# Kernel optimization log

Hardware: AMD Instinct MI355X
Metric: run time of the kernel (lower is better)

## Reference

```python
import jax, jax.numpy as jnp
import numpy as np
from jax import lax

NUM_GROUPS = 16
POOL_KS = 2
CLAMP_MIN = 0.0
CLAMP_MAX = 1.0
EPS = 1e-5


def setup_inputs() -> dict:
    key = jax.random.key(0)
    k1, k2, k3, k4, k5 = jax.random.split(key, 5)
    B, Cin, H, W = 32, 64, 128, 128
    Cout, K = 128, 3
    x = jax.random.normal(k1, (B, Cin, H, W), dtype=jnp.float32)
    fan_in = Cin * K * K
    bound = 1.0 / np.sqrt(fan_in)
    conv_w = jax.random.uniform(k2, (Cout, Cin, K, K), jnp.float32, -bound, bound)
    conv_b = jax.random.uniform(k3, (Cout,), jnp.float32, -bound, bound)
    gn_w = jnp.ones((Cout,), jnp.float32)
    gn_b = jnp.zeros((Cout,), jnp.float32)
    scale = jnp.ones((Cout, 1, 1), jnp.float32)
    return {"x": x, "conv_w": conv_w, "conv_b": conv_b,
            "gn_w": gn_w, "gn_b": gn_b, "scale": scale}


def reference(x, conv_w, conv_b, gn_w, gn_b, scale):
    # Conv2d, stride=1, padding=0  -> (B, Cout, Ho, Wo)
    y = lax.conv_general_dilated(
        x, conv_w, window_strides=(1, 1), padding="VALID",
        dimension_numbers=("NCHW", "OIHW", "NCHW"))
    y = y + conv_b[None, :, None, None]
    B, C, H, W = y.shape
    G = NUM_GROUPS
    # GroupNorm (biased variance, as in torch)
    yg = y.reshape(B, G, C // G, H, W)
    mean = jnp.mean(yg, axis=(2, 3, 4), keepdims=True)
    var = jnp.mean(jnp.square(yg), axis=(2, 3, 4), keepdims=True) - jnp.square(mean)
    yn = (yg - mean) * lax.rsqrt(var + EPS)
    yn = yn.reshape(B, C, H, W) * gn_w[None, :, None, None] + gn_b[None, :, None, None]
    # per-channel scale
    yn = yn * scale[None, :, :, :]
    # MaxPool2d(kernel=POOL_KS, stride=POOL_KS), VALID
    pooled = lax.reduce_window(
        yn, -jnp.inf, lax.max,
        window_dimensions=(1, 1, POOL_KS, POOL_KS),
        window_strides=(1, 1, POOL_KS, POOL_KS),
        padding="VALID")
    return jnp.clip(pooled, CLAMP_MIN, CLAMP_MAX)
```

## Files before the change

kernel.cpp:

```cpp
#include <hip/hip_runtime.h>
#include <stdint.h>
#include <stddef.h>

#define HIN 128
#define WIN 128
#define CINC 64
#define COUTC 128
#define HO 126
#define WO 126
#define HP 63
#define WP 63
#define NB 32
#define NG 16

typedef __bf16 bf16x8 __attribute__((ext_vector_type(8)));
typedef float f32x16 __attribute__((ext_vector_type(16)));

#define AS1U(p) ((const __attribute__((address_space(1))) unsigned int*)(p))
#define AS3U(p) ((__attribute__((address_space(3))) unsigned int*)(p))

__device__ __forceinline__ unsigned int f2bf(float f) {
  unsigned int u = __float_as_uint(f);
  return (u + 0x7fffu + ((u >> 16) & 1u)) >> 16;
}

__global__ __launch_bounds__(256) void wtrans_k(const float* __restrict__ w,
                                                unsigned short* __restrict__ wt2,
                                                float* __restrict__ stats) {
  int i = blockIdx.x * 256 + threadIdx.x;
  if (i < 1024) stats[i] = 0.0f;
  if (i >= 73728) return;
  int j = i & 7;
  int co = (i >> 3) & 127;
  int th = i >> 10;
  int half = th & 1, ks = (th >> 1) & 3, tap = th >> 3;
  int kh = tap / 3, kw = tap - 3 * kh;
  int cin = ks * 16 + half * 8 + j;
  float v = w[((co * CINC + cin) * 3 + kh) * 3 + kw];
  wt2[i] = (unsigned short)f2bf(v);
}

__global__ __launch_bounds__(256, 2) void conv_k(const float* __restrict__ x,
                                                 const unsigned short* __restrict__ wt2,
                                                 const float* __restrict__ conv_b,
                                                 float* __restrict__ out,
                                                 float* __restrict__ stats) {
  __shared__ __align__(16) unsigned int x_lds[18 * 18 * 32];
  __shared__ __align__(16) unsigned int aux_lds[8192];

  int t = threadIdx.x;
  int lane = t & 63, wave = t >> 6;
  int tw = blockIdx.x & 7, th = blockIdx.x >> 3;
  int b = blockIdx.y;
  int oh0 = th * 16, ow0 = tw * 16;
  int half = lane >> 5, m = lane & 31;

  int rot = (blockIdx.x + b) % 9;
  const unsigned int* wg = (const unsigned int*)wt2;

#define DMA_HALFTAP(j)                                                         \
  {                                                                            \
    int tapj = rot + ((j) >> 1);                                               \
    if (tapj >= 9) tapj -= 9;                                                  \
    int srcb = (tapj * 2 + ((j)&1)) * 2048;                                    \
    int slot = (j)&3;                                                          \
    _Pragma("unroll")                                                          \
    for (int jj = 0; jj < 2; ++jj) {                                           \
      int dof = jj * 1024 + wave * 256;                                        \
      __builtin_amdgcn_global_load_lds(AS1U(wg + srcb + dof + lane * 4),       \
                                       AS3U(&aux_lds[slot * 2048 + dof]), 16,  \
                                       0, 0);                                  \
    }                                                                          \
  }

  DMA_HALFTAP(0)
  DMA_HALFTAP(1)

  float bias[4];
#pragma unroll
  for (int nt = 0; nt < 4; ++nt) bias[nt] = conv_b[nt * 32 + m];

  const float* xb = x + (size_t)b * CINC * HIN * WIN;
#pragma unroll
  for (int k = 0; k < 12; ++k) {
    int i = k * 256 + t;
    if (i < 2880) {
      int c4 = i % 5;
      int j = i / 5;
      int p = j & 31;
      int r = j >> 5;
      int gr = oh0 + r;
      int gc0 = ow0 + c4 * 4;
      float4 v0 = make_float4(0.f, 0.f, 0.f, 0.f);
      float4 v1 = v0;
      if (gr < HIN && gc0 < WIN) {
        const float* base = xb + ((size_t)(2 * p) * HIN + gr) * WIN + gc0;
        v0 = *(const float4*)base;
        v1 = *(const float4*)(base + HIN * WIN);
      }
      float e0[4] = {v0.x, v0.y, v0.z, v0.w};
      float e1[4] = {v1.x, v1.y, v1.z, v1.w};
#pragma unroll
      for (int cc = 0; cc < 4; ++cc) {
        int c = c4 * 4 + cc;
        if (c < 18) {
          unsigned int d = f2bf(e0[cc]) | (f2bf(e1[cc]) << 16);
          x_lds[(r * 18 + c) * 32 + (p ^ ((c & 7) << 2))] = d;
        }
      }
    }
  }
  __syncthreads();

  f32x16 acc[2][4];
#pragma unroll
  for (int nt = 0; nt < 4; ++nt)
#pragma unroll
    for (int mt = 0; mt < 2; ++mt)
#pragma unroll
      for (int r = 0; r < 16; ++r) acc[mt][nt][r] = bias[nt];

  int prb = wave * 4 + (m >> 4);
  int pcc = m & 15;

#pragma unroll
  for (int i = 0; i < 18; ++i) {
    if (i + 2 < 18) DMA_HALFTAP(i + 2)

    int tap = rot + (i >> 1);
    if (tap >= 9) tap -= 9;
    int kh = (tap * 11) >> 5;
    int kw = tap - 3 * kh;
    int c = pcc + kw;
    int swz = (c & 7) << 2;
    int slot = i & 3;
    int hp = i & 1;
#pragma unroll
    for (int ks2 = 0; ks2 < 2; ++ks2) {
      int ks = hp * 2 + ks2;
      int ab = c * 32 + ((ks * 8 + half * 4) ^ swz);
      bf16x8 afr[2];
#pragma unroll
      for (int mt = 0; mt < 2; ++mt)
        afr[mt] = __builtin_bit_cast(
            bf16x8, *(const uint4*)&x_lds[(prb + mt * 2 + kh) * 576 + ab]);
      int wbase = slot * 2048 + ks2 * 1024 + half * 512 + m * 4;
      __builtin_amdgcn_s_setprio(1);
#pragma unroll
      for (int nt = 0; nt < 4; ++nt) {
        bf16x8 bfr =
            __builtin_bit_cast(bf16x8, *(const uint4*)&aux_lds[wbase + nt * 128]);
#pragma unroll
        for (int mt = 0; mt < 2; ++mt)
          acc[mt][nt] = __builtin_amdgcn_mfma_f32_32x32x16_bf16(
              afr[mt], bfr, acc[mt][nt], 0, 0, 0);
      }
      __builtin_amdgcn_s_setprio(0);
    }
    if (i < 16) {
      asm volatile("s_waitcnt vmcnt(2)" ::: "memory");
    } else if (i == 16) {
      asm volatile("s_waitcnt vmcnt(0)" ::: "memory");
    }
    if (i < 17) {
      __builtin_amdgcn_s_barrier();
      __builtin_amdgcn_sched_barrier(0);
    }
  }
#undef DMA_HALFTAP

  float s[4] = {0.f, 0.f, 0.f, 0.f}, qs[4] = {0.f, 0.f, 0.f, 0.f};
#pragma unroll
  for (int nt = 0; nt < 4; ++nt) {
#pragma unroll
    for (int mt = 0; mt < 2; ++mt) {
#pragma unroll
      for (int reg = 0; reg < 16; ++reg) {
        int c16 = (reg & 3) + 4 * half + 8 * ((reg >> 2) & 1);
        int r8 = wave * 4 + mt * 2 + (reg >> 3);
        if ((oh0 + r8) < HO && (ow0 + c16) < WO) {
          float v = acc[mt][nt][reg];
          s[nt] += v;
          qs[nt] += v * v;
        }
      }
    }
  }
#pragma unroll
  for (int nt = 0; nt < 4; ++nt) {
    float sv = s[nt], qv = qs[nt];
    sv += __shfl_xor(sv, 32);
    qv += __shfl_xor(qv, 32);
    sv += __shfl_down(sv, 4, 8);
    qv += __shfl_down(qv, 4, 8);
    sv += __shfl_down(sv, 2, 8);
    qv += __shfl_down(qv, 2, 8);
    sv += __shfl_down(sv, 1, 8);
    qv += __shfl_down(qv, 1, 8);
    if (half == 0 && (m & 7) == 0) {
      int g = nt * 4 + (m >> 3);
      atomicAdd(&stats[(b * NG + g) * 2 + 0], sv);
      atomicAdd(&stats[(b * NG + g) * 2 + 1], qv);
    }
  }

  __syncthreads();

#pragma unroll
  for (int nt = 0; nt < 4; ++nt) {
    int co = nt * 32 + m;
#pragma unroll
    for (int mt = 0; mt < 2; ++mt) {
      int oh2l = wave * 2 + mt;
#pragma unroll
      for (int i = 0; i < 4; ++i) {
        int r0 = 2 * i;
        int ow2l = (i & 1) + 2 * half + 4 * (i >> 1);
        float mx = fmaxf(fmaxf(acc[mt][nt][r0], acc[mt][nt][r0 + 1]),
                         fmaxf(acc[mt][nt][r0 + 8], acc[mt][nt][r0 + 9]));
        x_lds[co * 66 + oh2l * 8 + ow2l] = __float_as_uint(mx);
      }
    }
  }
  __syncthreads();

#pragma unroll
  for (int i = 0; i < 4; ++i) {
    int row = t * 4 + i;
    int co = row >> 3, oh2l = row & 7;
    int oh2 = th * 8 + oh2l;
    if (oh2 < HP) {
      const uint2* src = (const uint2*)&x_lds[co * 66 + oh2l * 8];
      uint2 d0 = src[0], d1 = src[1], d2 = src[2], d3 = src[3];
      unsigned int v[8] = {d0.x, d0.y, d1.x, d1.y, d2.x, d2.y, d3.x, d3.y};
      float* ob = out + ((size_t)(b * COUTC + co) * HP + oh2) * WP + tw * 8;
      int n = (tw == 7) ? 7 : 8;
#pragma unroll
      for (int e = 0; e < 8; ++e)
        if (e < n) ob[e] = __uint_as_float(v[e]);
    }
  }
}

__global__ __launch_bounds__(256) void fin_k(float* __restrict__ out,
                                             const float* __restrict__ stats,
                                             const float* __restrict__ gn_w,
                                             const float* __restrict__ gn_b,
                                             const float* __restrict__ scale) {
  const int plane = HP * WP;
  const float inv_cnt = 1.0f / (8.0f * HO * WO);
  int bc = blockIdx.x;
  int c = bc & 127, b = bc >> 7;
  int g = c >> 3;
  float su = stats[(b * NG + g) * 2 + 0];
  float sq = stats[(b * NG + g) * 2 + 1];
  float mean = su * inv_cnt;
  float var = fmaxf(sq * inv_cnt - mean * mean, 0.f);
  float rstd = rsqrtf(var + 1e-5f);
  float gw = gn_w[c], sc = scale[c];
  float A = rstd * gw * sc;
  float Bo = (gn_b[c] - mean * rstd * gw) * sc;

  float* p = out + (size_t)bc * plane;
  int t = threadIdx.x;
  int head = (4 - (bc & 3)) & 3;
  if (t < head) p[t] = fminf(fmaxf(fmaf(p[t], A, Bo), 0.0f), 1.0f);
  int n4 = (plane - head) >> 2;
  float4* p4 = (float4*)(p + head);
  for (int i = t; i < n4; i += 256) {
    float4 v = p4[i];
    v.x = fminf(fmaxf(fmaf(v.x, A, Bo), 0.0f), 1.0f);
    v.y = fminf(fmaxf(fmaf(v.y, A, Bo), 0.0f), 1.0f);
    v.z = fminf(fmaxf(fmaf(v.z, A, Bo), 0.0f), 1.0f);
    v.w = fminf(fmaxf(fmaf(v.w, A, Bo), 0.0f), 1.0f);
    p4[i] = v;
  }
  int done = head + (n4 << 2);
  int tail = plane - done;
  if (t < tail) p[done + t] = fminf(fmaxf(fmaf(p[done + t], A, Bo), 0.0f), 1.0f);
}

extern "C" void kernel_launch(void* const* d_in, const int* in_sizes, int n_in,
                              void* d_out, int out_size, void* d_ws, size_t ws_size,
                              hipStream_t stream) {
  const float* x      = (const float*)d_in[0];
  const float* conv_w = (const float*)d_in[1];
  const float* conv_b = (const float*)d_in[2];
  const float* gn_w   = (const float*)d_in[3];
  const float* gn_b   = (const float*)d_in[4];
  const float* scale  = (const float*)d_in[5];
  float* out = (float*)d_out;

  float* stats        = (float*)d_ws;
  unsigned short* wt2 = (unsigned short*)((char*)d_ws + 4096);

  wtrans_k<<<288, 256, 0, stream>>>(conv_w, wt2, stats);

  conv_k<<<dim3(64, NB), 256, 0, stream>>>(x, wt2, conv_b, out, stats);

  fin_k<<<4096, 256, 0, stream>>>(out, stats, gn_w, gn_b, scale);
}
```

Baseline: 379.4 us.

## Halve conv output tile height and split waves across channels for occupancy

Each conv block now covers an 8x16 output tile instead of 16x16. Its four waves are arranged as 2 row groups by 2 channel halves, so each wave accumulates 64 output channels instead of 128, and the grid doubles to 128x32 blocks. LDS per block shrinks (x tile of 10 rows, 4-slot weight ring at quarter-tap granularity with 36 pipeline steps) and launch bounds request 3 blocks per CU, aiming for higher occupancy and lower accumulator register pressure. The trade-offs are more halo re-reads of x, duplicated weight streaming per block, and a barrier on every one of the 36 steps.

```diff
diff --git a/kernel.cpp b/kernel.cpp
--- a/kernel.cpp
+++ b/kernel.cpp
@@ -40,51 +40,41 @@
   wt2[i] = (unsigned short)f2bf(v);
 }
 
-__global__ __launch_bounds__(256, 2) void conv_k(const float* __restrict__ x,
+__global__ __launch_bounds__(256, 3) void conv_k(const float* __restrict__ x,
                                                  const unsigned short* __restrict__ wt2,
                                                  const float* __restrict__ conv_b,
                                                  float* __restrict__ out,
                                                  float* __restrict__ stats) {
-  __shared__ __align__(16) unsigned int x_lds[18 * 18 * 32];
-  __shared__ __align__(16) unsigned int aux_lds[8192];
+  __shared__ __align__(16) unsigned int x_lds[10 * 18 * 32];
+  __shared__ __align__(16) unsigned int w_lds[4096];
 
   int t = threadIdx.x;
   int lane = t & 63, wave = t >> 6;
+  int wh = wave >> 1, wc = wave & 1;
   int tw = blockIdx.x & 7, th = blockIdx.x >> 3;
   int b = blockIdx.y;
-  int oh0 = th * 16, ow0 = tw * 16;
+  int oh0 = th * 8, ow0 = tw * 16;
   int half = lane >> 5, m = lane & 31;
-
-  int rot = (blockIdx.x + b) % 9;
+  int rot4 = (((int)blockIdx.x + b) % 9) * 4;
   const unsigned int* wg = (const unsigned int*)wt2;
 
-#define DMA_HALFTAP(j)                                                         \
-  {                                                                            \
-    int tapj = rot + ((j) >> 1);                                               \
-    if (tapj >= 9) tapj -= 9;                                                  \
-    int srcb = (tapj * 2 + ((j)&1)) * 2048;                                    \
-    int slot = (j)&3;                                                          \
-    _Pragma("unroll")                                                          \
-    for (int jj = 0; jj < 2; ++jj) {                                           \
-      int dof = jj * 1024 + wave * 256;                                        \
-      __builtin_amdgcn_global_load_lds(AS1U(wg + srcb + dof + lane * 4),       \
-                                       AS3U(&aux_lds[slot * 2048 + dof]), 16,  \
-                                       0, 0);                                  \
-    }                                                                          \
-  }
-
-  DMA_HALFTAP(0)
-  DMA_HALFTAP(1)
-
-  float bias[4];
-#pragma unroll
-  for (int nt = 0; nt < 4; ++nt) bias[nt] = conv_b[nt * 32 + m];
+#pragma unroll
+  for (int j = 0; j < 2; ++j) {
+    int rs = j + rot4;
+    if (rs >= 36) rs -= 36;
+    __builtin_amdgcn_global_load_lds(AS1U(wg + rs * 1024 + wave * 256 + lane * 4),
+                                     AS3U(&w_lds[j * 1024 + wave * 256]), 16, 0, 0);
+  }
+
+  float bias[2];
+#pragma unroll
+  for (int nt = 0; nt < 2; ++nt) bias[nt] = conv_b[wc * 64 + nt * 32 + m];
 
   const float* xb = x + (size_t)b * CINC * HIN * WIN;
 #pragma unroll
-  for (int k = 0; k < 12; ++k) {
+  for (int k = 0; k < 7; ++k) {
     int i = k * 256 + t;
-    if (i < 2880) {
+    if (i < 1600) {
       int c4 = i % 5;
       int j = i / 5;
       int p = j & 31;
@@ -112,72 +102,71 @@
   }
   __syncthreads();
 
-  f32x16 acc[2][4];
-#pragma unroll
-  for (int nt = 0; nt < 4; ++nt)
+  f32x16 acc[2][2];
+#pragma unroll
+  for (int nt = 0; nt < 2; ++nt)
 #pragma unroll
     for (int mt = 0; mt < 2; ++mt)
 #pragma unroll
       for (int r = 0; r < 16; ++r) acc[mt][nt][r] = bias[nt];
 
-  int prb = wave * 4 + (m >> 4);
+  int prb = wh * 4 + (m >> 4);
   int pcc = m & 15;
 
 #pragma unroll
-  for (int i = 0; i < 18; ++i) {
-    if (i + 2 < 18) DMA_HALFTAP(i + 2)
-
-    int tap = rot + (i >> 1);
-    if (tap >= 9) tap -= 9;
+  for (int j = 0; j < 36; ++j) {
+    if (j + 2 < 36) {
+      int rs2 = j + 2 + rot4;
+      if (rs2 >= 36) rs2 -= 36;
+      __builtin_amdgcn_global_load_lds(
+          AS1U(wg + rs2 * 1024 + wave * 256 + lane * 4),
+          AS3U(&w_lds[((j + 2) & 3) * 1024 + wave * 256]), 16, 0, 0);
+    }
+    if (j < 34)
+      asm volatile("s_waitcnt vmcnt(2)" ::: "memory");
+    else if (j == 34)
+      asm volatile("s_waitcnt vmcnt(1)" ::: "memory");
+    else
+      asm volatile("s_waitcnt vmcnt(0)" ::: "memory");
+    __builtin_amdgcn_s_barrier();
+    __builtin_amdgcn_sched_barrier(0);
+
+    int rs = j + rot4;
+    if (rs >= 36) rs -= 36;
+    int tap = rs >> 2;
+    const int ks = j & 3;
     int kh = (tap * 11) >> 5;
     int kw = tap - 3 * kh;
     int c = pcc + kw;
     int swz = (c & 7) << 2;
-    int slot = i & 3;
-    int hp = i & 1;
-#pragma unroll
-    for (int ks2 = 0; ks2 < 2; ++ks2) {
-      int ks = hp * 2 + ks2;
-      int ab = c * 32 + ((ks * 8 + half * 4) ^ swz);
-      bf16x8 afr[2];
+    int ab = c * 32 + ((ks * 8 + half * 4) ^ swz);
+    bf16x8 afr[2];
+#pragma unroll
+    for (int mt = 0; mt < 2; ++mt)
+      afr[mt] = __builtin_bit_cast(
+          bf16x8, *(const uint4*)&x_lds[(prb + mt * 2 + kh) * 576 + ab]);
+    int wb = (j & 3) * 1024 + half * 512 + wc * 256 + m * 4;
+    __builtin_amdgcn_s_setprio(1);
+#pragma unroll
+    for (int nt = 0; nt < 2; ++nt) {
+      bf16x8 bfr = __builtin_bit_cast(bf16x8, *(const uint4*)&w_lds[wb + nt * 128]);
 #pragma unroll
       for (int mt = 0; mt < 2; ++mt)
-        afr[mt] = __builtin_bit_cast(
-            bf16x8, *(const uint4*)&x_lds[(prb + mt * 2 + kh) * 576 + ab]);
-      int wbase = slot * 2048 + ks2 * 1024 + half * 512 + m * 4;
-      __builtin_amdgcn_s_setprio(1);
-#pragma unroll
-      for (int nt = 0; nt < 4; ++nt) {
-        bf16x8 bfr =
-            __builtin_bit_cast(bf16x8, *(const uint4*)&aux_lds[wbase + nt * 128]);
-#pragma unroll
-        for (int mt = 0; mt < 2; ++mt)
-          acc[mt][nt] = __builtin_amdgcn_mfma_f32_32x32x16_bf16(
-              afr[mt], bfr, acc[mt][nt], 0, 0, 0);
-      }
-      __builtin_amdgcn_s_setprio(0);
-    }
-    if (i < 16) {
-      asm volatile("s_waitcnt vmcnt(2)" ::: "memory");
-    } else if (i == 16) {
-      asm volatile("s_waitcnt vmcnt(0)" ::: "memory");
-    }
-    if (i < 17) {
-      __builtin_amdgcn_s_barrier();
-      __builtin_amdgcn_sched_barrier(0);
-    }
-  }
-#undef DMA_HALFTAP
-
-  float s[4] = {0.f, 0.f, 0.f, 0.f}, qs[4] = {0.f, 0.f, 0.f, 0.f};
-#pragma unroll
-  for (int nt = 0; nt < 4; ++nt) {
+        acc[mt][nt] = __builtin_amdgcn_mfma_f32_32x32x16_bf16(afr[mt], bfr,
+                                                              acc[mt][nt], 0, 0, 0);
+    }
+    __builtin_amdgcn_s_setprio(0);
+  }
+
+  float s[2] = {0.f, 0.f}, qs[2] = {0.f, 0.f};
+#pragma unroll
+  for (int nt = 0; nt < 2; ++nt) {
 #pragma unroll
     for (int mt = 0; mt < 2; ++mt) {
 #pragma unroll
       for (int reg = 0; reg < 16; ++reg) {
         int c16 = (reg & 3) + 4 * half + 8 * ((reg >> 2) & 1);
-        int r8 = wave * 4 + mt * 2 + (reg >> 3);
+        int r8 = wh * 4 + mt * 2 + (reg >> 3);
         if ((oh0 + r8) < HO && (ow0 + c16) < WO) {
           float v = acc[mt][nt][reg];
           s[nt] += v;
@@ -187,7 +176,7 @@
     }
   }
 #pragma unroll
-  for (int nt = 0; nt < 4; ++nt) {
+  for (int nt = 0; nt < 2; ++nt) {
     float sv = s[nt], qv = qs[nt];
     sv += __shfl_xor(sv, 32);
     qv += __shfl_xor(qv, 32);
@@ -198,7 +187,7 @@
     sv += __shfl_down(sv, 1, 8);
     qv += __shfl_down(qv, 1, 8);
     if (half == 0 && (m & 7) == 0) {
-      int g = nt * 4 + (m >> 3);
+      int g = wc * 8 + nt * 4 + (m >> 3);
       atomicAdd(&stats[(b * NG + g) * 2 + 0], sv);
       atomicAdd(&stats[(b * NG + g) * 2 + 1], qv);
     }
@@ -207,30 +196,30 @@
   __syncthreads();
 
 #pragma unroll
-  for (int nt = 0; nt < 4; ++nt) {
-    int co = nt * 32 + m;
+  for (int nt = 0; nt < 2; ++nt) {
+    int co = wc * 64 + nt * 32 + m;
 #pragma unroll
     for (int mt = 0; mt < 2; ++mt) {
-      int oh2l = wave * 2 + mt;
+      int oh2l = wh * 2 + mt;
 #pragma unroll
       for (int i = 0; i < 4; ++i) {
         int r0 = 2 * i;
         int ow2l = (i & 1) + 2 * half + 4 * (i >> 1);
         float mx = fmaxf(fmaxf(acc[mt][nt][r0], acc[mt][nt][r0 + 1]),
                          fmaxf(acc[mt][nt][r0 + 8], acc[mt][nt][r0 + 9]));
-        x_lds[co * 66 + oh2l * 8 + ow2l] = __float_as_uint(mx);
+        x_lds[co * 34 + oh2l * 8 + ow2l] = __float_as_uint(mx);
       }
     }
   }
   __syncthreads();
 
 #pragma unroll
-  for (int i = 0; i < 4; ++i) {
-    int row = t * 4 + i;
-    int co = row >> 3, oh2l = row & 7;
-    int oh2 = th * 8 + oh2l;
+  for (int i = 0; i < 2; ++i) {
+    int row = t * 2 + i;
+    int co = row >> 2, oh2l = row & 3;
+    int oh2 = th * 4 + oh2l;
     if (oh2 < HP) {
-      const uint2* src = (const uint2*)&x_lds[co * 66 + oh2l * 8];
+      const uint2* src = (const uint2*)&x_lds[co * 34 + oh2l * 8];
       uint2 d0 = src[0], d1 = src[1], d2 = src[2], d3 = src[3];
       unsigned int v[8] = {d0.x, d0.y, d1.x, d1.y, d2.x, d2.y, d3.x, d3.y};
       float* ob = out + ((size_t)(b * COUTC + co) * HP + oh2) * WP + tw * 8;
@@ -296,7 +285,7 @@
 
   wtrans_k<<<288, 256, 0, stream>>>(conv_w, wt2, stats);
 
-  conv_k<<<dim3(64, NB), 256, 0, stream>>>(x, wt2, conv_b, out, stats);
+  conv_k<<<dim3(128, NB), 256, 0, stream>>>(x, wt2, conv_b, out, stats);
 
   fin_k<<<4096, 256, 0, stream>>>(out, stats, gn_w, gn_b, scale);
 }
```

Result: no change. 382.5 us (+0.8%).
